# Optimization experiments

Hardware: AMD Instinct MI355X
Metric: run time of the kernel (lower is better)

Reference implementation:

```python
import jax, jax.numpy as jnp
import numpy as np

NEG_SLOPE = 0.2
EPS = 1e-16


def gat_layer(x, src, dst, Ws, Wd, a_s, a_d, b, heads, out_c, concat):
    # x: [N, F_in]; Ws/Wd: [F_in, heads*out_c]; a_s/a_d: [heads, out_c]; b: [heads*out_c] or [out_c]
    N = x.shape[0]
    xs = (x @ Ws).reshape(N, heads, out_c)  # src-projected features
    xd = (x @ Wd).reshape(N, heads, out_c)  # dst-projected features
    al_s = (xs * a_s).sum(-1)  # [N, H]
    al_d = (xd * a_d).sum(-1)  # [N, H]
    e = jax.nn.leaky_relu(al_s[src] + al_d[dst], negative_slope=NEG_SLOPE)  # [E, H]
    m = jax.ops.segment_max(e, dst, num_segments=N)  # [N, H], -inf for isolated nodes
    m = jnp.where(jnp.isfinite(m), m, 0.0)
    ex = jnp.exp(e - m[dst])
    den = jax.ops.segment_sum(ex, dst, num_segments=N)  # [N, H]
    alpha = ex / (den[dst] + EPS)  # segment softmax over incoming edges
    msg = xs[src] * alpha[:, :, None]  # [E, H, C]
    out = jax.ops.segment_sum(msg, dst, num_segments=N)  # [N, H, C]
    out = out.reshape(N, heads * out_c) if concat else out.mean(axis=1)
    return out + b


def setup_inputs() -> dict:
    key = jax.random.key(0)
    ks = jax.random.split(key, 20)
    N, E, F_in, H, Ch, Co = 50000, 400000, 128, 4, 128, 16
    s = lambda k, shp, fan: jax.random.normal(k, shp, dtype=jnp.float32) * (1.0 / np.sqrt(fan))
    inp = {
        "x": jax.random.normal(ks[0], (N, F_in), dtype=jnp.float32),
        "edge_index": jax.random.randint(ks[1], (2, E), 0, N, dtype=jnp.int32),
        # layer 1: in=128 -> heads=4, C=128, concat
        "Ws1": s(ks[2], (F_in, H * Ch), F_in), "Wd1": s(ks[3], (F_in, H * Ch), F_in),
        "as1": s(ks[4], (H, Ch), Ch), "ad1": s(ks[5], (H, Ch), Ch),
        "b1": jnp.zeros((H * Ch,), dtype=jnp.float32),
        # layer 2: in=512 -> heads=4, C=128, concat
        "Ws2": s(ks[6], (H * Ch, H * Ch), H * Ch), "Wd2": s(ks[7], (H * Ch, H * Ch), H * Ch),
        "as2": s(ks[8], (H, Ch), Ch), "ad2": s(ks[9], (H, Ch), Ch),
        "b2": jnp.zeros((H * Ch,), dtype=jnp.float32),
        # layer 3: in=512 -> heads=1, C=16, no concat
        "Ws3": s(ks[10], (H * Ch, Co), H * Ch), "Wd3": s(ks[11], (H * Ch, Co), H * Ch),
        "as3": s(ks[12], (1, Co), Co), "ad3": s(ks[13], (1, Co), Co),
        "b3": jnp.zeros((Co,), dtype=jnp.float32),
    }
    return inp


def reference(x, edge_index, Ws1, Wd1, as1, ad1, b1, Ws2, Wd2, as2, ad2, b2, Ws3, Wd3, as3, ad3, b3):
    src, dst = edge_index[0], edge_index[1]
    h = gat_layer(x, src, dst, Ws1, Wd1, as1, ad1, b1, heads=4, out_c=128, concat=True)
    h = jax.nn.relu(h)  # dropout = identity in eval mode
    h = gat_layer(h, src, dst, Ws2, Wd2, as2, ad2, b2, heads=4, out_c=128, concat=True)
    h = jax.nn.relu(h)
    out = gat_layer(h, src, dst, Ws3, Wd3, as3, ad3, b3, heads=1, out_c=16, concat=False)
    return out
```

## Files before the change

### kernel.cpp

```cpp
#include <hip/hip_runtime.h>
#include <math.h>

#define NEG_SLOPE 0.2f
#define EPSF 1e-16f

typedef _Float16 h2v __attribute__((ext_vector_type(2)));
typedef _Float16 h4v __attribute__((ext_vector_type(4)));
typedef _Float16 h8v __attribute__((ext_vector_type(8)));
typedef float f4v __attribute__((ext_vector_type(4)));

#define AS1 __attribute__((address_space(1)))
#define AS3 __attribute__((address_space(3)))

__device__ __forceinline__ void gll16(const void* g, void* l) {
  __builtin_amdgcn_global_load_lds((AS1 void*)g, (AS3 void*)l, 16, 0, 0);
}


__global__ void hist_kernel(const int* __restrict__ dst, int* __restrict__ counts, int E) {
  int t = blockIdx.x * 256 + threadIdx.x;
  if (t < E) atomicAdd(&counts[dst[t]], 1);
}

__global__ void scan1(const int* __restrict__ counts, int* __restrict__ offs,
                      int* __restrict__ bsum, int N) {
  __shared__ int sd[1024];
  int tid = threadIdx.x;
  int i = blockIdx.x * 1024 + tid;
  int v = (i < N) ? counts[i] : 0;
  sd[tid] = v;
  __syncthreads();
  for (int s = 1; s < 1024; s <<= 1) {
    int tv = (tid >= s) ? sd[tid - s] : 0;
    __syncthreads();
    sd[tid] += tv;
    __syncthreads();
  }
  if (i < N) offs[i] = sd[tid] - v;
  if (tid == 1023) bsum[blockIdx.x] = sd[1023];
}

__global__ void scan2(int* __restrict__ bsum, int* __restrict__ offs, int nb, int N, int E) {
  if (threadIdx.x == 0) {
    int r = 0;
    for (int i = 0; i < nb; i++) { int v = bsum[i]; bsum[i] = r; r += v; }
    offs[N] = E;
  }
}

__global__ void scan3(int* __restrict__ offs, const int* __restrict__ bsum, int N) {
  int i = blockIdx.x * 1024 + threadIdx.x;
  if (i < N) offs[i] += bsum[blockIdx.x];
}

__global__ void scatter_kernel(const int* __restrict__ src, const int* __restrict__ dst,
                               const int* __restrict__ off, int* __restrict__ cur,
                               int* __restrict__ srcp, int E) {
  int t = blockIdx.x * 256 + threadIdx.x;
  if (t < E) {
    int d = dst[t];
    int p = off[d] + atomicAdd(&cur[d], 1);
    srcp[p] = src[t];
  }
}


__global__ void convX(const float* __restrict__ x, _Float16* __restrict__ xh, int n4) {
  int i = blockIdx.x * 256 + threadIdx.x;
  if (i >= n4) return;
  float4 v = ((const float4*)x)[i];
  h4v h;
  h[0] = (_Float16)v.x; h[1] = (_Float16)v.y;
  h[2] = (_Float16)v.z; h[3] = (_Float16)v.w;
  ((h4v*)xh)[i] = h;
}

__global__ void convW(const float* __restrict__ W, _Float16* __restrict__ Th, int K) {
  __shared__ float tile[32][33];
  int bx = blockIdx.x * 32;
  int by = blockIdx.y * 32;
  int tx = threadIdx.x, ty = threadIdx.y;
#pragma unroll
  for (int i = 0; i < 32; i += 8)
    tile[ty + i][tx] = W[(size_t)(by + ty + i) * 512 + bx + tx];
  __syncthreads();
#pragma unroll
  for (int i = 0; i < 32; i += 8)
    Th[(size_t)(bx + ty + i) * K + by + tx] = (_Float16)tile[tx][ty + i];
}

__global__ void convW3(const float* __restrict__ W, _Float16* __restrict__ Th) {
  int t = blockIdx.x * 256 + threadIdx.x;
  if (t >= 512 * 16) return;
  int k = t >> 4, c = t & 15;
  Th[c * 512 + k] = (_Float16)W[t];
}


#define STAGE(bs, kt)                                  \
  do {                                                 \
    const size_t ko = (size_t)(kt) + w * 8;            \
    char* d0 = sm + (bs) + (w * 128) * 16;             \
    char* d1 = d0 + 1024;                              \
    gll16(A + (tm + l) * K + ko,      d0);             \
    gll16(A + (tm + 64 + l) * K + ko, d1);             \
    gll16(Bh + (cn + l) * K + ko,      d0 + 8192);     \
    gll16(Bh + (cn + 64 + l) * K + ko, d1 + 8192);     \
  } while (0)

template <int K>
__global__ __launch_bounds__(256) void gemm_f16(
    const _Float16* __restrict__ A, const _Float16* __restrict__ Bh,
    const float* __restrict__ a_s, _Float16* __restrict__ C,
    float* __restrict__ als, int M) {
  __shared__ __align__(16) char sm[49152];
  const int t = threadIdx.x;
  const int w = t >> 6, l = t & 63;
  const int wr = w >> 1, wc = w & 1;
  const int kg = l >> 4, rr = l & 15;

  const int nwg = gridDim.x;
  const int q = nwg >> 3, r = nwg & 7;
  const int orig = blockIdx.x;
  const int xcd = orig & 7, slot = orig >> 3;
  const int wgid = (xcd < r ? xcd * (q + 1) : r * (q + 1) + (xcd - r) * q) + slot;
  const size_t tm = (size_t)(wgid >> 2) * 128;
  const size_t cn = (size_t)(wgid & 3) * 128;

  f4v acc[4][4];
#pragma unroll
  for (int i = 0; i < 4; i++)
#pragma unroll
    for (int j = 0; j < 4; j++) acc[i][j] = (f4v){0.f, 0.f, 0.f, 0.f};

  STAGE(0, 0);
  STAGE(16384, 32);
  int o_cur = 0, o_nxt = 16384, o_3rd = 32768;

#pragma unroll 4
  for (int kt = 0; kt < K; kt += 32) {
    if (kt + 32 < K) {
      asm volatile("s_waitcnt vmcnt(4)" ::: "memory");
    } else {
      asm volatile("s_waitcnt vmcnt(0)" ::: "memory");
    }
    __builtin_amdgcn_sched_barrier(0);
    __builtin_amdgcn_s_barrier();
    if (kt + 64 < K) STAGE(o_3rd, kt + 64);

    const char* base = sm + o_cur;
    h8v ah[4], bh[4];
#pragma unroll
    for (int i = 0; i < 4; i++) {
      int ca = (kg * 128 + wr * 64 + i * 16 + rr) * 16;
      int cb = (kg * 128 + wc * 64 + i * 16 + rr) * 16;
      ah[i] = *(const h8v*)(base + ca);
      bh[i] = *(const h8v*)(base + 8192 + cb);
    }
#pragma unroll
    for (int i = 0; i < 4; i++)
#pragma unroll
      for (int j = 0; j < 4; j++)
        acc[i][j] = __builtin_amdgcn_mfma_f32_16x16x32_f16(ah[i], bh[j], acc[i][j], 0, 0, 0);

    int tmp = o_cur; o_cur = o_nxt; o_nxt = o_3rd; o_3rd = tmp;
  }

  float sp[16];
#pragma unroll
  for (int k = 0; k < 16; k++) sp[k] = 0.f;
#pragma unroll
  for (int i = 0; i < 4; i++) {
    int row0 = wr * 64 + i * 16 + kg * 4;
#pragma unroll
    for (int j = 0; j < 4; j++) {
      int col = wc * 64 + j * 16 + rr;
      float aw = a_s[cn + col];
#pragma unroll
      for (int r2 = 0; r2 < 4; r2++) {
        float v = acc[i][j][r2];
        size_t row = tm + row0 + r2;
        if (row < (size_t)M) C[row * 512 + cn + col] = (_Float16)v;
        sp[i * 4 + r2] += v * aw;
      }
    }
  }
#pragma unroll
  for (int o = 1; o < 16; o <<= 1)
#pragma unroll
    for (int k = 0; k < 16; k++) sp[k] += __shfl_xor(sp[k], o);
  __syncthreads();
  float* ap = (float*)sm;
  if (wc == 0 && rr == 0) {
#pragma unroll
    for (int k = 0; k < 16; k++)
      ap[wr * 64 + (k >> 2) * 16 + kg * 4 + (k & 3)] = sp[k];
  }
  __syncthreads();
  if (wc == 1 && rr == 0) {
    int head = (int)(cn >> 7);
#pragma unroll
    for (int k = 0; k < 16; k++) {
      int row = wr * 64 + (k >> 2) * 16 + kg * 4 + (k & 3);
      size_t grow = tm + row;
      if (grow < (size_t)M) als[grow * 4 + head] = ap[row] + sp[k];
    }
  }
}


__global__ __launch_bounds__(256) void gemm3(const _Float16* __restrict__ A,
                                             const _Float16* __restrict__ Bth,
                                             const float* __restrict__ as3,
                                             float* __restrict__ C,
                                             float* __restrict__ als, int M) {
  int wv = threadIdx.x >> 6, l = threadIdx.x & 63;
  size_t tm = ((size_t)blockIdx.x * 4 + wv) * 16;
  if (tm >= (size_t)M) return;
  int rr = l & 15, kg = l >> 4;
  f4v acc = (f4v){0.f, 0.f, 0.f, 0.f};
  for (int kt = 0; kt < 512; kt += 32) {
    int ka = kt + kg * 8;
    h8v a_h = *(const h8v*)&A[(tm + rr) * 512 + ka];
    h8v b_h = *(const h8v*)&Bth[rr * 512 + ka];
    acc = __builtin_amdgcn_mfma_f32_16x16x32_f16(a_h, b_h, acc, 0, 0, 0);
  }
  float aw = as3[rr];
  float s[4];
#pragma unroll
  for (int r = 0; r < 4; r++) s[r] = acc[r] * aw;
#pragma unroll
  for (int o = 1; o < 16; o <<= 1)
#pragma unroll
    for (int r = 0; r < 4; r++) s[r] += __shfl_xor(s[r], o);
#pragma unroll
  for (int r = 0; r < 4; r++) {
    size_t row = tm + kg * 4 + r;
    if (row < (size_t)M) {
      C[row * 16 + rr] = acc[r];
      if (rr == 0) als[row] = s[r];
    }
  }
}


__global__ void wsd_kernel(const float* __restrict__ Wd, const float* __restrict__ a_d,
                           float* __restrict__ wsd, int K, int H, int C) {
  int g = (blockIdx.x * 256 + threadIdx.x) >> 4;
  int l16 = threadIdx.x & 15;
  if (g >= K * H) return;
  int k = g / H, h = g - k * H;
  int ce = C >> 4;
  float s = 0.f;
  for (int j = 0; j < ce; j++) {
    int c = l16 * ce + j;
    s += Wd[(size_t)k * (H * C) + h * C + c] * a_d[h * C + c];
  }
#pragma unroll
  for (int o = 1; o < 16; o <<= 1) s += __shfl_xor(s, o);
  if (l16 == 0) wsd[k * H + h] = s;
}


template <int K>
__global__ void wgt4_kernel(const float* __restrict__ als, const _Float16* __restrict__ hin,
                            const float* __restrict__ wsd, const int* __restrict__ off,
                            const int* __restrict__ srcp, _Float16* __restrict__ wgt, int N) {
  int wid = threadIdx.x >> 6, lane = threadIdx.x & 63;
  int n = blockIdx.x * 4 + wid;
  if (n >= N) return;
  int p0 = off[n], deg = off[n + 1] - p0;
  if (deg == 0) return;

  float d0 = 0.f, d1 = 0.f, d2 = 0.f, d3 = 0.f;
  constexpr int KP = K / 64;
  {
    int k0 = lane * KP;
    if constexpr (K == 512) {
      h8v qv = *(const h8v*)&hin[(size_t)n * K + k0];
#pragma unroll
      for (int j = 0; j < 8; j++) {
        float xv = (float)qv[j];
        float4 wv = *(const float4*)&wsd[(k0 + j) * 4];
        d0 += xv * wv.x; d1 += xv * wv.y; d2 += xv * wv.z; d3 += xv * wv.w;
      }
    } else {
      h2v qv = *(const h2v*)&hin[(size_t)n * K + k0];
#pragma unroll
      for (int j = 0; j < KP; j++) {
        float xv = (float)qv[j];
        float4 wv = *(const float4*)&wsd[(k0 + j) * 4];
        d0 += xv * wv.x; d1 += xv * wv.y; d2 += xv * wv.z; d3 += xv * wv.w;
      }
    }
#pragma unroll
    for (int o = 1; o < 64; o <<= 1) {
      d0 += __shfl_xor(d0, o); d1 += __shfl_xor(d1, o);
      d2 += __shfl_xor(d2, o); d3 += __shfl_xor(d3, o);
    }
  }
  int h = lane & 3, e = lane >> 2;
  float aldn = (h == 0) ? d0 : (h == 1) ? d1 : (h == 2) ? d2 : d3;

  float ev0 = -1e30f;
  if (e < deg) {
    float v = als[srcp[p0 + e] * 4 + h] + aldn;
    ev0 = (v > 0.f) ? v : NEG_SLOPE * v;
  }
  float m = ev0;
  for (int base = 16; base < deg; base += 16) {
    float ev = -1e30f;
    if (base + e < deg) {
      float v = als[srcp[p0 + base + e] * 4 + h] + aldn;
      ev = (v > 0.f) ? v : NEG_SLOPE * v;
    }
    m = fmaxf(m, ev);
  }
#pragma unroll
  for (int o = 4; o < 64; o <<= 1) m = fmaxf(m, __shfl_xor(m, o));
  float den = (e < deg) ? __expf(ev0 - m) : 0.f;
  for (int base = 16; base < deg; base += 16) {
    if (base + e < deg) {
      float v = als[srcp[p0 + base + e] * 4 + h] + aldn;
      v = (v > 0.f) ? v : NEG_SLOPE * v;
      den += __expf(v - m);
    }
  }
#pragma unroll
  for (int o = 4; o < 64; o <<= 1) den += __shfl_xor(den, o);
  float rw = 1.f / (den + EPSF);
  if (e < deg) wgt[(size_t)(p0 + e) * 4 + h] = (_Float16)(__expf(ev0 - m) * rw);
  for (int base = 16; base < deg; base += 16) {
    if (base + e < deg) {
      float v = als[srcp[p0 + base + e] * 4 + h] + aldn;
      v = (v > 0.f) ? v : NEG_SLOPE * v;
      wgt[(size_t)(p0 + base + e) * 4 + h] = (_Float16)(__expf(v - m) * rw);
    }
  }
}

__global__ void wgt1_kernel(const float* __restrict__ als, const _Float16* __restrict__ hin,
                            const float* __restrict__ wsd, const int* __restrict__ off,
                            const int* __restrict__ srcp, _Float16* __restrict__ wgt, int N) {
  int wid = threadIdx.x >> 6, lane = threadIdx.x & 63;
  int n = blockIdx.x * 4 + wid;
  if (n >= N) return;
  int p0 = off[n], deg = off[n + 1] - p0;
  if (deg == 0) return;

  float aldn = 0.f;
  {
    h8v qv = *(const h8v*)&hin[(size_t)n * 512 + lane * 8];
#pragma unroll
    for (int j = 0; j < 8; j++) aldn += (float)qv[j] * wsd[lane * 8 + j];
#pragma unroll
    for (int o = 1; o < 64; o <<= 1) aldn += __shfl_xor(aldn, o);
  }

  float ev0 = -1e30f;
  if (lane < deg) {
    float v = als[srcp[p0 + lane]] + aldn;
    ev0 = (v > 0.f) ? v : NEG_SLOPE * v;
  }
  float m = ev0;
  for (int base = 64; base < deg; base += 64) {
    float ev = -1e30f;
    if (base + lane < deg) {
      float v = als[srcp[p0 + base + lane]] + aldn;
      ev = (v > 0.f) ? v : NEG_SLOPE * v;
    }
    m = fmaxf(m, ev);
  }
#pragma unroll
  for (int o = 1; o < 64; o <<= 1) m = fmaxf(m, __shfl_xor(m, o));
  float den = (lane < deg) ? __expf(ev0 - m) : 0.f;
  for (int base = 64; base < deg; base += 64) {
    if (base + lane < deg) {
      float v = als[srcp[p0 + base + lane]] + aldn;
      v = (v > 0.f) ? v : NEG_SLOPE * v;
      den += __expf(v - m);
    }
  }
#pragma unroll
  for (int o = 1; o < 64; o <<= 1) den += __shfl_xor(den, o);
  float rw = 1.f / (den + EPSF);
  if (lane < deg) wgt[p0 + lane] = (_Float16)(__expf(ev0 - m) * rw);
  for (int base = 64; base < deg; base += 64) {
    if (base + lane < deg) {
      float v = als[srcp[p0 + base + lane]] + aldn;
      v = (v > 0.f) ? v : NEG_SLOPE * v;
      wgt[p0 + base + lane] = (_Float16)(__expf(v - m) * rw);
    }
  }
}


__global__ __launch_bounds__(128) void agg512(
    const _Float16* __restrict__ xs, const _Float16* __restrict__ wgt,
    const int* __restrict__ off, const int* __restrict__ srcp,
    const float* __restrict__ bias, _Float16* __restrict__ oh, int N) {
  int n = blockIdx.x;
  int t = threadIdx.x;
  int h = t >> 5;
  int p0 = off[n], p1 = off[n + 1];
  float a0 = 0.f, a1 = 0.f, a2 = 0.f, a3 = 0.f;
  float c0 = 0.f, c1 = 0.f, c2 = 0.f, c3 = 0.f;
  int p = p0;
  for (; p + 1 < p1; p += 2) {
    int s0 = srcp[p], s1 = srcp[p + 1];
    float w0 = (float)wgt[(size_t)p * 4 + h];
    float w1 = (float)wgt[(size_t)(p + 1) * 4 + h];
    h4v v0 = *(const h4v*)&xs[(size_t)s0 * 512 + 4 * t];
    h4v v1 = *(const h4v*)&xs[(size_t)s1 * 512 + 4 * t];
    a0 += w0 * (float)v0[0]; a1 += w0 * (float)v0[1];
    a2 += w0 * (float)v0[2]; a3 += w0 * (float)v0[3];
    c0 += w1 * (float)v1[0]; c1 += w1 * (float)v1[1];
    c2 += w1 * (float)v1[2]; c3 += w1 * (float)v1[3];
  }
  if (p < p1) {
    int s0 = srcp[p];
    float w0 = (float)wgt[(size_t)p * 4 + h];
    h4v v0 = *(const h4v*)&xs[(size_t)s0 * 512 + 4 * t];
    a0 += w0 * (float)v0[0]; a1 += w0 * (float)v0[1];
    a2 += w0 * (float)v0[2]; a3 += w0 * (float)v0[3];
  }
  a0 += c0; a1 += c1; a2 += c2; a3 += c3;
  float4 b = *(const float4*)&bias[4 * t];
  a0 = fmaxf(a0 + b.x, 0.f); a1 = fmaxf(a1 + b.y, 0.f);
  a2 = fmaxf(a2 + b.z, 0.f); a3 = fmaxf(a3 + b.w, 0.f);
  h4v wh;
  wh[0] = (_Float16)a0; wh[1] = (_Float16)a1;
  wh[2] = (_Float16)a2; wh[3] = (_Float16)a3;
  *(h4v*)&oh[(size_t)n * 512 + 4 * t] = wh;
}

__global__ void agg16(const float* __restrict__ xs3, const _Float16* __restrict__ wgt,
                      const int* __restrict__ off, const int* __restrict__ srcp,
                      const float* __restrict__ bias, float* __restrict__ out, int N) {
  int g = threadIdx.x >> 4, c = threadIdx.x & 15;
  int n = blockIdx.x * 16 + g;
  if (n >= N) return;
  int p0 = off[n], p1 = off[n + 1];
  float acc = 0.f;
  for (int p = p0; p < p1; p++)
    acc += (float)wgt[p] * xs3[(size_t)srcp[p] * 16 + c];
  out[(size_t)n * 16 + c] = acc + bias[c];
}


extern "C" void kernel_launch(void* const* d_in, const int* in_sizes, int n_in,
                              void* d_out, int out_size, void* d_ws, size_t ws_size,
                              hipStream_t stream) {
  const float* x   = (const float*)d_in[0];
  const int*   ei  = (const int*)d_in[1];
  const float* Ws1 = (const float*)d_in[2];
  const float* Wd1 = (const float*)d_in[3];
  const float* as1 = (const float*)d_in[4];
  const float* ad1 = (const float*)d_in[5];
  const float* b1  = (const float*)d_in[6];
  const float* Ws2 = (const float*)d_in[7];
  const float* Wd2 = (const float*)d_in[8];
  const float* as2 = (const float*)d_in[9];
  const float* ad2 = (const float*)d_in[10];
  const float* b2  = (const float*)d_in[11];
  const float* Ws3 = (const float*)d_in[12];
  const float* Wd3 = (const float*)d_in[13];
  const float* as3 = (const float*)d_in[14];
  const float* ad3 = (const float*)d_in[15];
  const float* b3  = (const float*)d_in[16];

  const int N = in_sizes[0] / 128;
  const int E = in_sizes[1] / 2;
  const int* src = ei;
  const int* dst = ei + E;

  char* w = (char*)d_ws;
  _Float16* xs     = (_Float16*)(w + 0);
  _Float16* hbuf   = (_Float16*)(w + 51200000);
  float*    als    = (float*)(w + 102400000);
  float*    xs3    = (float*)(w + 104000000);
  _Float16* wgt    = (_Float16*)(w + 107200000);
  int*      counts = (int*)(w + 110400000);
  int*      cur    = (int*)(w + 110600000);
  int*      offs   = (int*)(w + 110800000);
  int*      bsum   = (int*)(w + 111000192);
  int*      srcp   = (int*)(w + 111004288);
  float*    wsd    = (float*)(w + 112604288);
  _Float16* wt_hi  = (_Float16*)(w + 112612480);
  _Float16* wt3_hi = (_Float16*)(w + 113136768);

  hipMemsetAsync(counts, 0, 2 * (size_t)N * 4, stream);
  hist_kernel<<<(E + 255) / 256, 256, 0, stream>>>(dst, counts, E);
  int nb = (N + 1023) / 1024;
  scan1<<<nb, 1024, 0, stream>>>(counts, offs, bsum, N);
  scan2<<<1, 64, 0, stream>>>(bsum, offs, nb, N, E);
  scan3<<<nb, 1024, 0, stream>>>(offs, bsum, N);
  scatter_kernel<<<(E + 255) / 256, 256, 0, stream>>>(src, dst, offs, cur, srcp, E);

  int ggrid = ((N + 127) / 128) * 4;
  dim3 cwb(32, 8);
  int nwb = (N + 3) / 4;

  convX<<<(N * 128 / 4 + 255) / 256, 256, 0, stream>>>(x, hbuf, N * 128 / 4);
  wsd_kernel<<<(128 * 4 * 16 + 255) / 256, 256, 0, stream>>>(Wd1, ad1, wsd, 128, 4, 128);
  convW<<<dim3(16, 4), cwb, 0, stream>>>(Ws1, wt_hi, 128);
  gemm_f16<128><<<ggrid, 256, 0, stream>>>(hbuf, wt_hi, as1, xs, als, N);
  wgt4_kernel<128><<<nwb, 256, 0, stream>>>(als, hbuf, wsd, offs, srcp, wgt, N);
  agg512<<<N, 128, 0, stream>>>(xs, wgt, offs, srcp, b1, hbuf, N);

  wsd_kernel<<<(512 * 4 * 16 + 255) / 256, 256, 0, stream>>>(Wd2, ad2, wsd, 512, 4, 128);
  convW<<<dim3(16, 16), cwb, 0, stream>>>(Ws2, wt_hi, 512);
  gemm_f16<512><<<ggrid, 256, 0, stream>>>(hbuf, wt_hi, as2, xs, als, N);
  wgt4_kernel<512><<<nwb, 256, 0, stream>>>(als, hbuf, wsd, offs, srcp, wgt, N);
  agg512<<<N, 128, 0, stream>>>(xs, wgt, offs, srcp, b2, hbuf, N);

  wsd_kernel<<<(512 * 16 + 255) / 256, 256, 0, stream>>>(Wd3, ad3, wsd, 512, 1, 16);
  convW3<<<32, 256, 0, stream>>>(Ws3, wt3_hi);
  gemm3<<<(N / 16 + 4) / 4, 256, 0, stream>>>(hbuf, wt3_hi, as3, xs3, als, N);
  wgt1_kernel<<<nwb, 256, 0, stream>>>(als, hbuf, wsd, offs, srcp, wgt, N);
  agg16<<<(N + 15) / 16, 256, 0, stream>>>(xs3, wgt, offs, srcp, b3, (float*)d_out, N);
}
```

Before: 512.9 us.

## Restructure f16 GEMM into 256x64 tiles with register-resident A and swizzled LDS B

The projection GEMM now uses 256x64 output tiles. Each wave loads its 64 rows of A straight into registers, double-buffered, while only B goes through a 3-stage XOR-swizzled LDS ring. This cuts shared memory from 48KB to 12KB and drops the LDS round-trip for A. The attention-score partial sums are now written as 8 per-strip values per row instead of being combined per head through LDS, so the weight kernel sums two adjacent partials per head when it reads them. The cost is that each A row is fetched from global memory by 8 column strips, which leans on L2 for reuse, and the grid is remapped across XCDs with a simpler formula.

```diff
diff --git a/kernel.cpp b/kernel.cpp
--- a/kernel.cpp
+++ b/kernel.cpp
@@ -97,35 +97,31 @@
 }
 
 
-#define STAGE(bs, kt)                                  \
-  do {                                                 \
-    const size_t ko = (size_t)(kt) + w * 8;            \
-    char* d0 = sm + (bs) + (w * 128) * 16;             \
-    char* d1 = d0 + 1024;                              \
-    gll16(A + (tm + l) * K + ko,      d0);             \
-    gll16(A + (tm + 64 + l) * K + ko, d1);             \
-    gll16(Bh + (cn + l) * K + ko,      d0 + 8192);     \
-    gll16(Bh + (cn + 64 + l) * K + ko, d1 + 8192);     \
-  } while (0)
-
 template <int K>
 __global__ __launch_bounds__(256) void gemm_f16(
     const _Float16* __restrict__ A, const _Float16* __restrict__ Bh,
     const float* __restrict__ a_s, _Float16* __restrict__ C,
-    float* __restrict__ als, int M) {
-  __shared__ __align__(16) char sm[49152];
+    float* __restrict__ als8, int M) {
+  __shared__ __align__(16) char sm[12288];
+  constexpr int T = K / 32;
   const int t = threadIdx.x;
   const int w = t >> 6, l = t & 63;
-  const int wr = w >> 1, wc = w & 1;
   const int kg = l >> 4, rr = l & 15;
 
   const int nwg = gridDim.x;
-  const int q = nwg >> 3, r = nwg & 7;
   const int orig = blockIdx.x;
-  const int xcd = orig & 7, slot = orig >> 3;
-  const int wgid = (xcd < r ? xcd * (q + 1) : r * (q + 1) + (xcd - r) * q) + slot;
-  const size_t tm = (size_t)(wgid >> 2) * 128;
-  const size_t cn = (size_t)(wgid & 3) * 128;
+  const int wgid = (orig & 7) * (nwg >> 3) + (orig >> 3);
+  const size_t tm = (size_t)(wgid >> 3) * 256;
+  const int strip = wgid & 7;
+  const size_t cn = (size_t)strip * 64;
+
+  const size_t arow = tm + (size_t)w * 64;
+
+  const int br = t >> 2;
+  const int bkp = (t & 3) ^ (br & 3) ^ ((br >> 2) & 3);
+  const _Float16* bsrc = Bh + (cn + br) * K + bkp * 8;
+  char* bdst = sm + t * 16;
+  const int bslot = kg ^ (rr & 3) ^ ((rr >> 2) & 3);
 
   f4v acc[4][4];
 #pragma unroll
@@ -133,37 +129,47 @@
 #pragma unroll
     for (int j = 0; j < 4; j++) acc[i][j] = (f4v){0.f, 0.f, 0.f, 0.f};
 
-  STAGE(0, 0);
-  STAGE(16384, 32);
-  int o_cur = 0, o_nxt = 16384, o_3rd = 32768;
-
-#pragma unroll 4
-  for (int kt = 0; kt < K; kt += 32) {
-    if (kt + 32 < K) {
-      asm volatile("s_waitcnt vmcnt(4)" ::: "memory");
+  h8v a0[4], a1[4];
+  gll16(bsrc, bdst);
+#pragma unroll
+  for (int i = 0; i < 4; i++)
+    a0[i] = *(const h8v*)&A[(arow + i * 16 + rr) * K + kg * 8];
+  gll16(bsrc + 32, bdst + 4096);
+#pragma unroll
+  for (int i = 0; i < 4; i++)
+    a1[i] = *(const h8v*)&A[(arow + i * 16 + rr) * K + 32 + kg * 8];
+
+#pragma unroll
+  for (int ts = 0; ts < T; ts++) {
+    const int kt = ts * 32;
+    if (ts + 1 < T) {
+      asm volatile("s_waitcnt vmcnt(5)" ::: "memory");
     } else {
       asm volatile("s_waitcnt vmcnt(0)" ::: "memory");
     }
     __builtin_amdgcn_sched_barrier(0);
     __builtin_amdgcn_s_barrier();
-    if (kt + 64 < K) STAGE(o_3rd, kt + 64);
-
-    const char* base = sm + o_cur;
-    h8v ah[4], bh[4];
-#pragma unroll
-    for (int i = 0; i < 4; i++) {
-      int ca = (kg * 128 + wr * 64 + i * 16 + rr) * 16;
-      int cb = (kg * 128 + wc * 64 + i * 16 + rr) * 16;
-      ah[i] = *(const h8v*)(base + ca);
-      bh[i] = *(const h8v*)(base + 8192 + cb);
-    }
+
+    if (ts + 2 < T) gll16(bsrc + kt + 64, sm + ((ts + 2) % 3) * 4096 + t * 16);
+
+    const char* base = sm + (ts % 3) * 4096;
+    h8v bf[4];
+#pragma unroll
+    for (int j = 0; j < 4; j++)
+      bf[j] = *(const h8v*)(base + (j * 16 + rr) * 64 + bslot * 16);
+
+    h8v(&ar)[4] = (ts & 1) ? a1 : a0;
 #pragma unroll
     for (int i = 0; i < 4; i++)
 #pragma unroll
       for (int j = 0; j < 4; j++)
-        acc[i][j] = __builtin_amdgcn_mfma_f32_16x16x32_f16(ah[i], bh[j], acc[i][j], 0, 0, 0);
-
-    int tmp = o_cur; o_cur = o_nxt; o_nxt = o_3rd; o_3rd = tmp;
+        acc[i][j] = __builtin_amdgcn_mfma_f32_16x16x32_f16(ar[i], bf[j], acc[i][j], 0, 0, 0);
+
+    if (ts + 2 < T) {
+#pragma unroll
+      for (int i = 0; i < 4; i++)
+        ar[i] = *(const h8v*)&A[(arow + i * 16 + rr) * K + kt + 64 + kg * 8];
+    }
   }
 
   float sp[16];
@@ -171,15 +177,14 @@
   for (int k = 0; k < 16; k++) sp[k] = 0.f;
 #pragma unroll
   for (int i = 0; i < 4; i++) {
-    int row0 = wr * 64 + i * 16 + kg * 4;
 #pragma unroll
     for (int j = 0; j < 4; j++) {
-      int col = wc * 64 + j * 16 + rr;
+      int col = j * 16 + rr;
       float aw = a_s[cn + col];
 #pragma unroll
       for (int r2 = 0; r2 < 4; r2++) {
         float v = acc[i][j][r2];
-        size_t row = tm + row0 + r2;
+        size_t row = arow + i * 16 + kg * 4 + r2;
         if (row < (size_t)M) C[row * 512 + cn + col] = (_Float16)v;
         sp[i * 4 + r2] += v * aw;
       }
@@ -189,21 +194,11 @@
   for (int o = 1; o < 16; o <<= 1)
 #pragma unroll
     for (int k = 0; k < 16; k++) sp[k] += __shfl_xor(sp[k], o);
-  __syncthreads();
-  float* ap = (float*)sm;
-  if (wc == 0 && rr == 0) {
-#pragma unroll
-    for (int k = 0; k < 16; k++)
-      ap[wr * 64 + (k >> 2) * 16 + kg * 4 + (k & 3)] = sp[k];
-  }
-  __syncthreads();
-  if (wc == 1 && rr == 0) {
-    int head = (int)(cn >> 7);
+  if (rr == 0) {
 #pragma unroll
     for (int k = 0; k < 16; k++) {
-      int row = wr * 64 + (k >> 2) * 16 + kg * 4 + (k & 3);
-      size_t grow = tm + row;
-      if (grow < (size_t)M) als[grow * 4 + head] = ap[row] + sp[k];
+      size_t row = arow + (k >> 2) * 16 + kg * 4 + (k & 3);
+      if (row < (size_t)M) als8[row * 8 + strip] = sp[k];
     }
   }
 }
@@ -262,8 +257,13 @@
 }
 
 
+__device__ __forceinline__ float als4(const float* __restrict__ a8, int s, int h) {
+  float2 v = *(const float2*)&a8[(size_t)s * 8 + 2 * h];
+  return v.x + v.y;
+}
+
 template <int K>
-__global__ void wgt4_kernel(const float* __restrict__ als, const _Float16* __restrict__ hin,
+__global__ void wgt4_kernel(const float* __restrict__ als8, const _Float16* __restrict__ hin,
                             const float* __restrict__ wsd, const int* __restrict__ off,
                             const int* __restrict__ srcp, _Float16* __restrict__ wgt, int N) {
   int wid = threadIdx.x >> 6, lane = threadIdx.x & 63;
@@ -304,14 +304,14 @@
 
   float ev0 = -1e30f;
   if (e < deg) {
-    float v = als[srcp[p0 + e] * 4 + h] + aldn;
+    float v = als4(als8, srcp[p0 + e], h) + aldn;
     ev0 = (v > 0.f) ? v : NEG_SLOPE * v;
   }
   float m = ev0;
   for (int base = 16; base < deg; base += 16) {
     float ev = -1e30f;
     if (base + e < deg) {
-      float v = als[srcp[p0 + base + e] * 4 + h] + aldn;
+      float v = als4(als8, srcp[p0 + base + e], h) + aldn;
       ev = (v > 0.f) ? v : NEG_SLOPE * v;
     }
     m = fmaxf(m, ev);
@@ -321,7 +321,7 @@
   float den = (e < deg) ? __expf(ev0 - m) : 0.f;
   for (int base = 16; base < deg; base += 16) {
     if (base + e < deg) {
-      float v = als[srcp[p0 + base + e] * 4 + h] + aldn;
+      float v = als4(als8, srcp[p0 + base + e], h) + aldn;
       v = (v > 0.f) ? v : NEG_SLOPE * v;
       den += __expf(v - m);
     }
@@ -332,7 +332,7 @@
   if (e < deg) wgt[(size_t)(p0 + e) * 4 + h] = (_Float16)(__expf(ev0 - m) * rw);
   for (int base = 16; base < deg; base += 16) {
     if (base + e < deg) {
-      float v = als[srcp[p0 + base + e] * 4 + h] + aldn;
+      float v = als4(als8, srcp[p0 + base + e], h) + aldn;
       v = (v > 0.f) ? v : NEG_SLOPE * v;
       wgt[(size_t)(p0 + base + e) * 4 + h] = (_Float16)(__expf(v - m) * rw);
     }
@@ -477,7 +477,7 @@
   char* w = (char*)d_ws;
   _Float16* xs     = (_Float16*)(w + 0);
   _Float16* hbuf   = (_Float16*)(w + 51200000);
-  float*    als    = (float*)(w + 102400000);
+  float*    als8   = (float*)(w + 102400000);
   float*    xs3    = (float*)(w + 104000000);
   _Float16* wgt    = (_Float16*)(w + 107200000);
   int*      counts = (int*)(w + 110400000);
@@ -497,26 +497,26 @@
   scan3<<<nb, 1024, 0, stream>>>(offs, bsum, N);
   scatter_kernel<<<(E + 255) / 256, 256, 0, stream>>>(src, dst, offs, cur, srcp, E);
 
-  int ggrid = ((N + 127) / 128) * 4;
+  int ggrid = ((N + 255) / 256) * 8;
   dim3 cwb(32, 8);
   int nwb = (N + 3) / 4;
 
   convX<<<(N * 128 / 4 + 255) / 256, 256, 0, stream>>>(x, hbuf, N * 128 / 4);
   wsd_kernel<<<(128 * 4 * 16 + 255) / 256, 256, 0, stream>>>(Wd1, ad1, wsd, 128, 4, 128);
   convW<<<dim3(16, 4), cwb, 0, stream>>>(Ws1, wt_hi, 128);
-  gemm_f16<128><<<ggrid, 256, 0, stream>>>(hbuf, wt_hi, as1, xs, als, N);
-  wgt4_kernel<128><<<nwb, 256, 0, stream>>>(als, hbuf, wsd, offs, srcp, wgt, N);
+  gemm_f16<128><<<ggrid, 256, 0, stream>>>(hbuf, wt_hi, as1, xs, als8, N);
+  wgt4_kernel<128><<<nwb, 256, 0, stream>>>(als8, hbuf, wsd, offs, srcp, wgt, N);
   agg512<<<N, 128, 0, stream>>>(xs, wgt, offs, srcp, b1, hbuf, N);
 
   wsd_kernel<<<(512 * 4 * 16 + 255) / 256, 256, 0, stream>>>(Wd2, ad2, wsd, 512, 4, 128);
   convW<<<dim3(16, 16), cwb, 0, stream>>>(Ws2, wt_hi, 512);
-  gemm_f16<512><<<ggrid, 256, 0, stream>>>(hbuf, wt_hi, as2, xs, als, N);
-  wgt4_kernel<512><<<nwb, 256, 0, stream>>>(als, hbuf, wsd, offs, srcp, wgt, N);
+  gemm_f16<512><<<ggrid, 256, 0, stream>>>(hbuf, wt_hi, as2, xs, als8, N);
+  wgt4_kernel<512><<<nwb, 256, 0, stream>>>(als8, hbuf, wsd, offs, srcp, wgt, N);
   agg512<<<N, 128, 0, stream>>>(xs, wgt, offs, srcp, b2, hbuf, N);
 
   wsd_kernel<<<(512 * 16 + 255) / 256, 256, 0, stream>>>(Wd3, ad3, wsd, 512, 1, 16);
   convW3<<<32, 256, 0, stream>>>(Ws3, wt3_hi);
-  gemm3<<<(N / 16 + 4) / 4, 256, 0, stream>>>(hbuf, wt3_hi, as3, xs3, als, N);
-  wgt1_kernel<<<nwb, 256, 0, stream>>>(als, hbuf, wsd, offs, srcp, wgt, N);
+  gemm3<<<(N / 16 + 4) / 4, 256, 0, stream>>>(hbuf, wt3_hi, as3, xs3, als8, N);
+  wgt1_kernel<<<nwb, 256, 0, stream>>>(als8, hbuf, wsd, offs, srcp, wgt, N);
   agg16<<<(N + 15) / 16, 256, 0, stream>>>(xs3, wgt, offs, srcp, b3, (float*)d_out, N);
 }
```

Result: no change. 518.7 us (+1.1%).

## Fuse next-layer dst attention logits into aggregation and stage GEMM output via LDS

Applied to the files above, without the earlier changes.

The dot product of each node's aggregated features with the precomputed Wd·a_d vector for the next layer now runs inside agg512, which writes al_d per node. The layer-2 and layer-3 weight kernels then read that value instead of re-reading the 512-wide hidden row. Separately, the GEMM epilogue stages the fp16 tile in shared memory and writes rows back with 16-byte vector stores in place of scattered 2-byte stores. This adds LDS use and an extra barrier in the GEMM, plus a shuffle reduction and a block sync in every aggregation block.

```diff
diff --git a/kernel.cpp b/kernel.cpp
--- a/kernel.cpp
+++ b/kernel.cpp
@@ -170,33 +170,48 @@
 #pragma unroll
   for (int k = 0; k < 16; k++) sp[k] = 0.f;
 #pragma unroll
+  for (int i = 0; i < 4; i++)
+#pragma unroll
+    for (int j = 0; j < 4; j++) {
+      float aw = a_s[cn + wc * 64 + j * 16 + rr];
+#pragma unroll
+      for (int r2 = 0; r2 < 4; r2++) sp[i * 4 + r2] += acc[i][j][r2] * aw;
+    }
+#pragma unroll
+  for (int o = 1; o < 16; o <<= 1)
+#pragma unroll
+    for (int k = 0; k < 16; k++) sp[k] += __shfl_xor(sp[k], o);
+
+  __syncthreads();
+  _Float16* ct = (_Float16*)sm;
+#pragma unroll
   for (int i = 0; i < 4; i++) {
     int row0 = wr * 64 + i * 16 + kg * 4;
 #pragma unroll
     for (int j = 0; j < 4; j++) {
       int col = wc * 64 + j * 16 + rr;
-      float aw = a_s[cn + col];
-#pragma unroll
-      for (int r2 = 0; r2 < 4; r2++) {
-        float v = acc[i][j][r2];
-        size_t row = tm + row0 + r2;
-        if (row < (size_t)M) C[row * 512 + cn + col] = (_Float16)v;
-        sp[i * 4 + r2] += v * aw;
-      }
-    }
-  }
-#pragma unroll
-  for (int o = 1; o < 16; o <<= 1)
-#pragma unroll
-    for (int k = 0; k < 16; k++) sp[k] += __shfl_xor(sp[k], o);
-  __syncthreads();
-  float* ap = (float*)sm;
+#pragma unroll
+      for (int r2 = 0; r2 < 4; r2++) ct[(row0 + r2) * 136 + col] = (_Float16)acc[i][j][r2];
+    }
+  }
+  float* ap = (float*)(sm + 34816);
   if (wc == 0 && rr == 0) {
 #pragma unroll
     for (int k = 0; k < 16; k++)
       ap[wr * 64 + (k >> 2) * 16 + kg * 4 + (k & 3)] = sp[k];
   }
   __syncthreads();
+  {
+    int row = t >> 1, half = t & 1;
+    size_t grow = tm + row;
+    if (grow < (size_t)M) {
+      const _Float16* srow = ct + row * 136 + half * 64;
+      _Float16* drow = C + grow * 512 + cn + half * 64;
+#pragma unroll
+      for (int qq = 0; qq < 8; qq++)
+        *(h8v*)(drow + qq * 8) = *(const h8v*)(srow + qq * 8);
+    }
+  }
   if (wc == 1 && rr == 0) {
     int head = (int)(cn >> 7);
 #pragma unroll
@@ -262,7 +277,6 @@
 }
 
 
-template <int K>
 __global__ void wgt4_kernel(const float* __restrict__ als, const _Float16* __restrict__ hin,
                             const float* __restrict__ wsd, const int* __restrict__ off,
                             const int* __restrict__ srcp, _Float16* __restrict__ wgt, int N) {
@@ -273,25 +287,14 @@
   if (deg == 0) return;
 
   float d0 = 0.f, d1 = 0.f, d2 = 0.f, d3 = 0.f;
-  constexpr int KP = K / 64;
   {
-    int k0 = lane * KP;
-    if constexpr (K == 512) {
-      h8v qv = *(const h8v*)&hin[(size_t)n * K + k0];
-#pragma unroll
-      for (int j = 0; j < 8; j++) {
-        float xv = (float)qv[j];
-        float4 wv = *(const float4*)&wsd[(k0 + j) * 4];
-        d0 += xv * wv.x; d1 += xv * wv.y; d2 += xv * wv.z; d3 += xv * wv.w;
-      }
-    } else {
-      h2v qv = *(const h2v*)&hin[(size_t)n * K + k0];
-#pragma unroll
-      for (int j = 0; j < KP; j++) {
-        float xv = (float)qv[j];
-        float4 wv = *(const float4*)&wsd[(k0 + j) * 4];
-        d0 += xv * wv.x; d1 += xv * wv.y; d2 += xv * wv.z; d3 += xv * wv.w;
-      }
+    int k0 = lane * 2;
+    h2v qv = *(const h2v*)&hin[(size_t)n * 128 + k0];
+#pragma unroll
+    for (int j = 0; j < 2; j++) {
+      float xv = (float)qv[j];
+      float4 wv = *(const float4*)&wsd[(k0 + j) * 4];
+      d0 += xv * wv.x; d1 += xv * wv.y; d2 += xv * wv.z; d3 += xv * wv.w;
     }
 #pragma unroll
     for (int o = 1; o < 64; o <<= 1) {
@@ -339,23 +342,63 @@
   }
 }
 
-__global__ void wgt1_kernel(const float* __restrict__ als, const _Float16* __restrict__ hin,
-                            const float* __restrict__ wsd, const int* __restrict__ off,
-                            const int* __restrict__ srcp, _Float16* __restrict__ wgt, int N) {
+__global__ void wgt4p_kernel(const float* __restrict__ als, const float* __restrict__ ald,
+                             const int* __restrict__ off, const int* __restrict__ srcp,
+                             _Float16* __restrict__ wgt, int N) {
   int wid = threadIdx.x >> 6, lane = threadIdx.x & 63;
   int n = blockIdx.x * 4 + wid;
   if (n >= N) return;
   int p0 = off[n], deg = off[n + 1] - p0;
   if (deg == 0) return;
-
-  float aldn = 0.f;
-  {
-    h8v qv = *(const h8v*)&hin[(size_t)n * 512 + lane * 8];
-#pragma unroll
-    for (int j = 0; j < 8; j++) aldn += (float)qv[j] * wsd[lane * 8 + j];
-#pragma unroll
-    for (int o = 1; o < 64; o <<= 1) aldn += __shfl_xor(aldn, o);
-  }
+  int h = lane & 3, e = lane >> 2;
+  float aldn = ald[n * 4 + h];
+
+  float ev0 = -1e30f;
+  if (e < deg) {
+    float v = als[srcp[p0 + e] * 4 + h] + aldn;
+    ev0 = (v > 0.f) ? v : NEG_SLOPE * v;
+  }
+  float m = ev0;
+  for (int base = 16; base < deg; base += 16) {
+    float ev = -1e30f;
+    if (base + e < deg) {
+      float v = als[srcp[p0 + base + e] * 4 + h] + aldn;
+      ev = (v > 0.f) ? v : NEG_SLOPE * v;
+    }
+    m = fmaxf(m, ev);
+  }
+#pragma unroll
+  for (int o = 4; o < 64; o <<= 1) m = fmaxf(m, __shfl_xor(m, o));
+  float den = (e < deg) ? __expf(ev0 - m) : 0.f;
+  for (int base = 16; base < deg; base += 16) {
+    if (base + e < deg) {
+      float v = als[srcp[p0 + base + e] * 4 + h] + aldn;
+      v = (v > 0.f) ? v : NEG_SLOPE * v;
+      den += __expf(v - m);
+    }
+  }
+#pragma unroll
+  for (int o = 4; o < 64; o <<= 1) den += __shfl_xor(den, o);
+  float rw = 1.f / (den + EPSF);
+  if (e < deg) wgt[(size_t)(p0 + e) * 4 + h] = (_Float16)(__expf(ev0 - m) * rw);
+  for (int base = 16; base < deg; base += 16) {
+    if (base + e < deg) {
+      float v = als[srcp[p0 + base + e] * 4 + h] + aldn;
+      v = (v > 0.f) ? v : NEG_SLOPE * v;
+      wgt[(size_t)(p0 + base + e) * 4 + h] = (_Float16)(__expf(v - m) * rw);
+    }
+  }
+}
+
+__global__ void wgt1p_kernel(const float* __restrict__ als, const float* __restrict__ ald,
+                             const int* __restrict__ off, const int* __restrict__ srcp,
+                             _Float16* __restrict__ wgt, int N) {
+  int wid = threadIdx.x >> 6, lane = threadIdx.x & 63;
+  int n = blockIdx.x * 4 + wid;
+  if (n >= N) return;
+  int p0 = off[n], deg = off[n + 1] - p0;
+  if (deg == 0) return;
+  float aldn = ald[n];
 
   float ev0 = -1e30f;
   if (lane < deg) {
@@ -395,10 +438,13 @@
 }
 
 
+template <int HN>
 __global__ __launch_bounds__(128) void agg512(
     const _Float16* __restrict__ xs, const _Float16* __restrict__ wgt,
     const int* __restrict__ off, const int* __restrict__ srcp,
-    const float* __restrict__ bias, _Float16* __restrict__ oh, int N) {
+    const float* __restrict__ bias, const float* __restrict__ wsdn,
+    _Float16* __restrict__ oh, float* __restrict__ aldo, int N) {
+  __shared__ float red[8];
   int n = blockIdx.x;
   int t = threadIdx.x;
   int h = t >> 5;
@@ -432,6 +478,42 @@
   wh[0] = (_Float16)a0; wh[1] = (_Float16)a1;
   wh[2] = (_Float16)a2; wh[3] = (_Float16)a3;
   *(h4v*)&oh[(size_t)n * 512 + 4 * t] = wh;
+
+  if constexpr (HN == 4) {
+    float4 w0 = ((const float4*)wsdn)[4 * t + 0];
+    float4 w1 = ((const float4*)wsdn)[4 * t + 1];
+    float4 w2 = ((const float4*)wsdn)[4 * t + 2];
+    float4 w3 = ((const float4*)wsdn)[4 * t + 3];
+    float p0h = a0 * w0.x + a1 * w1.x + a2 * w2.x + a3 * w3.x;
+    float p1h = a0 * w0.y + a1 * w1.y + a2 * w2.y + a3 * w3.y;
+    float p2h = a0 * w0.z + a1 * w1.z + a2 * w2.z + a3 * w3.z;
+    float p3h = a0 * w0.w + a1 * w1.w + a2 * w2.w + a3 * w3.w;
+#pragma unroll
+    for (int o = 1; o < 64; o <<= 1) {
+      p0h += __shfl_xor(p0h, o); p1h += __shfl_xor(p1h, o);
+      p2h += __shfl_xor(p2h, o); p3h += __shfl_xor(p3h, o);
+    }
+    if ((t & 63) == 0) {
+      int wv = t >> 6;
+      red[wv * 4 + 0] = p0h; red[wv * 4 + 1] = p1h;
+      red[wv * 4 + 2] = p2h; red[wv * 4 + 3] = p3h;
+    }
+    __syncthreads();
+    if (t == 0) {
+      float4 rr;
+      rr.x = red[0] + red[4]; rr.y = red[1] + red[5];
+      rr.z = red[2] + red[6]; rr.w = red[3] + red[7];
+      *(float4*)&aldo[(size_t)n * 4] = rr;
+    }
+  } else if constexpr (HN == 1) {
+    float4 wv4 = *(const float4*)&wsdn[4 * t];
+    float ph = a0 * wv4.x + a1 * wv4.y + a2 * wv4.z + a3 * wv4.w;
+#pragma unroll
+    for (int o = 1; o < 64; o <<= 1) ph += __shfl_xor(ph, o);
+    if ((t & 63) == 0) red[t >> 6] = ph;
+    __syncthreads();
+    if (t == 0) aldo[n] = red[0] + red[1];
+  }
 }
 
 __global__ void agg16(const float* __restrict__ xs3, const _Float16* __restrict__ wgt,
@@ -478,6 +560,7 @@
   _Float16* xs     = (_Float16*)(w + 0);
   _Float16* hbuf   = (_Float16*)(w + 51200000);
   float*    als    = (float*)(w + 102400000);
+  float*    ald    = (float*)(w + 103200000);
   float*    xs3    = (float*)(w + 104000000);
   _Float16* wgt    = (_Float16*)(w + 107200000);
   int*      counts = (int*)(w + 110400000);
@@ -485,9 +568,11 @@
   int*      offs   = (int*)(w + 110800000);
   int*      bsum   = (int*)(w + 111000192);
   int*      srcp   = (int*)(w + 111004288);
-  float*    wsd    = (float*)(w + 112604288);
-  _Float16* wt_hi  = (_Float16*)(w + 112612480);
-  _Float16* wt3_hi = (_Float16*)(w + 113136768);
+  float*    wsd1   = (float*)(w + 112604288);
+  float*    wsd2   = (float*)(w + 112606336);
+  float*    wsd3   = (float*)(w + 112614528);
+  _Float16* wt_hi  = (_Float16*)(w + 112616576);
+  _Float16* wt3_hi = (_Float16*)(w + 113140864);
 
   hipMemsetAsync(counts, 0, 2 * (size_t)N * 4, stream);
   hist_kernel<<<(E + 255) / 256, 256, 0, stream>>>(dst, counts, E);
@@ -501,22 +586,23 @@
   dim3 cwb(32, 8);
   int nwb = (N + 3) / 4;
 
+  wsd_kernel<<<(128 * 4 * 16 + 255) / 256, 256, 0, stream>>>(Wd1, ad1, wsd1, 128, 4, 128);
+  wsd_kernel<<<(512 * 4 * 16 + 255) / 256, 256, 0, stream>>>(Wd2, ad2, wsd2, 512, 4, 128);
+  wsd_kernel<<<(512 * 16 + 255) / 256, 256, 0, stream>>>(Wd3, ad3, wsd3, 512, 1, 16);
+
   convX<<<(N * 128 / 4 + 255) / 256, 256, 0, stream>>>(x, hbuf, N * 128 / 4);
-  wsd_kernel<<<(128 * 4 * 16 + 255) / 256, 256, 0, stream>>>(Wd1, ad1, wsd, 128, 4, 128);
   convW<<<dim3(16, 4), cwb, 0, stream>>>(Ws1, wt_hi, 128);
   gemm_f16<128><<<ggrid, 256, 0, stream>>>(hbuf, wt_hi, as1, xs, als, N);
-  wgt4_kernel<128><<<nwb, 256, 0, stream>>>(als, hbuf, wsd, offs, srcp, wgt, N);
-  agg512<<<N, 128, 0, stream>>>(xs, wgt, offs, srcp, b1, hbuf, N);
-
-  wsd_kernel<<<(512 * 4 * 16 + 255) / 256, 256, 0, stream>>>(Wd2, ad2, wsd, 512, 4, 128);
+  wgt4_kernel<<<nwb, 256, 0, stream>>>(als, hbuf, wsd1, offs, srcp, wgt, N);
+  agg512<4><<<N, 128, 0, stream>>>(xs, wgt, offs, srcp, b1, wsd2, hbuf, ald, N);
+
   convW<<<dim3(16, 16), cwb, 0, stream>>>(Ws2, wt_hi, 512);
   gemm_f16<512><<<ggrid, 256, 0, stream>>>(hbuf, wt_hi, as2, xs, als, N);
-  wgt4_kernel<512><<<nwb, 256, 0, stream>>>(als, hbuf, wsd, offs, srcp, wgt, N);
-  agg512<<<N, 128, 0, stream>>>(xs, wgt, offs, srcp, b2, hbuf, N);
-
-  wsd_kernel<<<(512 * 16 + 255) / 256, 256, 0, stream>>>(Wd3, ad3, wsd, 512, 1, 16);
+  wgt4p_kernel<<<nwb, 256, 0, stream>>>(als, ald, offs, srcp, wgt, N);
+  agg512<1><<<N, 128, 0, stream>>>(xs, wgt, offs, srcp, b2, wsd3, hbuf, ald, N);
+
   convW3<<<32, 256, 0, stream>>>(Ws3, wt3_hi);
   gemm3<<<(N / 16 + 4) / 4, 256, 0, stream>>>(hbuf, wt3_hi, as3, xs3, als, N);
-  wgt1_kernel<<<nwb, 256, 0, stream>>>(als, hbuf, wsd, offs, srcp, wgt, N);
+  wgt1p_kernel<<<nwb, 256, 0, stream>>>(als, ald, offs, srcp, wgt, N);
   agg16<<<(N + 15) / 16, 256, 0, stream>>>(xs3, wgt, offs, srcp, b3, (float*)d_out, N);
 }
```

Result: faster. 489.5 us (-4.6%).
